# Kernel tuning notes

Measured on AMD Instinct MI355X. Metric: run time of the kernel, lower is better.

The kernel has to match this reference:

```python
import jax, jax.numpy as jnp
import numpy as np

DEPTH = 3
WIDTH = 512
WIDTH_SUB = 256
B = 64
L = 512
EPS = 1e-5
C_IN = 2 * WIDTH_SUB  # == WIDTH here, so per-depth params stack uniformly


def setup_inputs() -> dict:
    key = jax.random.key(0)
    ks = jax.random.split(key, 4)
    s = 1.0 / np.sqrt(C_IN).astype(np.float32)
    P_matrix = jax.random.normal(ks[0], (B, C_IN, L), jnp.float32)
    Wq = jax.random.normal(ks[1], (DEPTH, WIDTH, C_IN), jnp.float32) * s
    Wk = jax.random.normal(ks[2], (DEPTH, WIDTH, C_IN), jnp.float32) * s
    Wv = jax.random.normal(ks[3], (DEPTH, WIDTH, C_IN), jnp.float32) * s
    zeros = jnp.zeros((DEPTH, WIDTH), jnp.float32)
    ones = jnp.ones((DEPTH, WIDTH), jnp.float32)
    return {
        "P_matrix": P_matrix,
        "Wq": Wq, "bq": zeros, "gq": ones, "betaq": zeros,
        "Wk": Wk, "bk": zeros, "gk": ones, "betak": zeros,
        "Wv": Wv, "bv": zeros, "gv": ones, "betav": zeros,
    }


def _ncl_linear(x, W, b, gamma, beta):
    # x: [B, C, L]; Linear over channel dim, then BatchNorm1d (training stats) + ReLU
    y = jnp.einsum('bcl,oc->bol', x, W) + b[None, :, None]  # [B, O, L]
    mean = y.mean(axis=(0, 2), keepdims=True)
    var = y.var(axis=(0, 2), keepdims=True)  # biased, as torch BN uses for normalization
    y = (y - mean) * jax.lax.rsqrt(var + EPS) * gamma[None, :, None] + beta[None, :, None]
    return jax.nn.relu(y)


def reference(P_matrix, Wq, bq, gq, betaq, Wk, bk, gk, betak, Wv, bv, gv, betav):
    x = P_matrix
    for i in range(DEPTH):
        Q = _ncl_linear(x, Wq[i], bq[i], gq[i], betaq[i])  # [B, W, L]
        K = _ncl_linear(x, Wk[i], bk[i], gk[i], betak[i])
        V = _ncl_linear(x, Wv[i], bv[i], gv[i], betav[i])
        w = jnp.einsum('bcl,bdl->bcd', Q, K)  # [B, W, W], unscaled
        # nn.Softmax() with dim=None on a 3D tensor -> dim=0 in torch
        a = jax.nn.softmax(w, axis=0)
        x = jnp.einsum('bcd,bdl->bcl', a, V)  # [B, W, L]
    return x
```

## Files before the change

### kernel.cpp

```cpp
#include <hip/hip_runtime.h>
#include <hip/hip_fp8.h>
#include <stdint.h>

typedef __bf16 bf16_t;
typedef bf16_t bf16x8 __attribute__((ext_vector_type(8)));
typedef bf16_t bf16x4 __attribute__((ext_vector_type(4)));
typedef float  f32x4  __attribute__((ext_vector_type(4)));

#define MFMA_BF16(a,b,c) __builtin_amdgcn_mfma_f32_16x16x32_bf16(a,b,c,0,0,0)

__device__ __forceinline__ void load_lds16(const bf16_t* g, bf16_t* l) {
  __builtin_amdgcn_global_load_lds((const __attribute__((address_space(1))) void*)g,
                                   (__attribute__((address_space(3))) void*)l,
                                   16, 0, 0);
}

__device__ __forceinline__ float fp8_to_f(uint8_t b) {
  return (float)__builtin_bit_cast(__hip_fp8_e4m3, b);
}
__device__ __forceinline__ uint8_t f_to_fp8(float f) {
  return __builtin_bit_cast(uint8_t, __hip_fp8_e4m3(f));
}
__device__ __forceinline__ uint8_t fp8s_enc(float r) { return f_to_fp8(r * 256.f); }
__device__ __forceinline__ float   fp8s_dec(uint8_t b) { return fp8_to_f(b) * (1.f/256.f); }

__global__ __launch_bounds__(256) void cast_w_kern(const float* __restrict__ wq,
    const float* __restrict__ wk, const float* __restrict__ wv,
    bf16_t* __restrict__ whi, bf16_t* __restrict__ wlo) {
  const int i = blockIdx.x * 256 + threadIdx.x;
  const int idx = i * 4;
  const int p = idx / 786432;
  const int r = idx - p * 786432;
  const float* s = (p == 0 ? wq : (p == 1 ? wk : wv));
  float4 v = *(const float4*)(s + r);
  float f[4] = {v.x, v.y, v.z, v.w};
  bf16x4 hi, lo;
#pragma unroll
  for (int j = 0; j < 4; ++j) {
    bf16_t h = (bf16_t)f[j];
    hi[j] = h;
    lo[j] = (bf16_t)(f[j] - (float)h);
  }
  const size_t o = (size_t)p * 786432 + r;
  *(bf16x4*)(whi + o) = hi;
  *(bf16x4*)(wlo + o) = lo;
}

__global__ __launch_bounds__(256) void transpose_split_in_kern(
    const float* __restrict__ P, bf16_t* __restrict__ xh, uint8_t* __restrict__ xl) {
  __shared__ float t[32][33];
  const int bz = blockIdx.x >> 8;
  const int ti = blockIdx.x & 255;
  const int tc = (ti >> 4) * 32;
  const int tl = (ti & 15) * 32;
  const float* Pb = P + (size_t)bz * 262144;
  bf16_t* xb = xh + (size_t)bz * 262144;
  uint8_t* lb = xl + (size_t)bz * 262144;
  const int tx = threadIdx.x & 31, ty = threadIdx.x >> 5;
#pragma unroll
  for (int k = 0; k < 4; ++k)
    t[ty*4+k][tx] = Pb[(size_t)(tc + ty*4 + k)*512 + tl + tx];
  __syncthreads();
#pragma unroll
  for (int k = 0; k < 4; ++k) {
    const float f = t[tx][ty*4+k];
    const bf16_t h = (bf16_t)f;
    const size_t o = (size_t)(tl + ty*4 + k)*512 + tc + tx;
    xb[o] = h;
    lb[o] = fp8s_enc(f - (float)h);
  }
}

__global__ __launch_bounds__(256) void gemm_qkv_kern(
    const bf16_t* __restrict__ Whi, const bf16_t* __restrict__ Wlo,
    const bf16_t* __restrict__ xh, const uint8_t* __restrict__ xl,
    const float* __restrict__ bq, const float* __restrict__ bk,
    const float* __restrict__ bv, int depth,
    bf16_t* __restrict__ Qh, uint8_t* __restrict__ Ql,
    bf16_t* __restrict__ Kh, uint8_t* __restrict__ Kl,
    bf16_t* __restrict__ Yvh, bf16_t* __restrict__ Yvl) {
  __shared__ __align__(16) bf16_t Ah[4096], Al[4096], Bh[4096], Bl[4096];
  const int blk = blockIdx.x;
  const int t  = blk & 15;
  const int pb = blk >> 4;
  const int b  = pb & 63, p = pb >> 6;
  const int row0 = (t >> 2) * 128, col0 = (t & 3) * 128;
  const size_t woff = (size_t)p * 786432 + (size_t)depth * 262144;
  const bf16_t* A_hi = Whi + woff;
  const bf16_t* A_lo = Wlo + woff;
  const bf16_t* B_hi = xh + (size_t)b * 262144;
  const uint8_t* B_lo = xl + (size_t)b * 262144;
  const int tid = threadIdx.x, lane = tid & 63, wid = tid >> 6;
  const int wm = wid >> 1, wn = wid & 1;
  const int sr = tid >> 2, scs = (tid & 3) * 8;
  const int frow = lane & 15, fk = (lane >> 4) * 8;
  const int lrow = tid >> 1, lhalf = (tid & 1) * 16;
  f32x4 acc[4][4] = {};
  bf16_t* lah = Ah + wid * 512;
  bf16_t* lal = Al + wid * 512;
  bf16_t* lbh = Bh + wid * 512;
  const bf16_t* gah = A_hi + (size_t)(row0 + sr) * 512 + scs;
  const bf16_t* gal = A_lo + (size_t)(row0 + sr) * 512 + scs;
  const bf16_t* gbh = B_hi + (size_t)(col0 + sr) * 512 + scs;
  const uint8_t* gbl = B_lo + (size_t)(col0 + lrow) * 512 + lhalf;
  for (int ks = 0; ks < 16; ++ks) {
    const int k0 = ks * 32;
    load_lds16(gah + k0, lah); load_lds16(gah + 32768 + k0, lah + 2048);
    load_lds16(gal + k0, lal); load_lds16(gal + 32768 + k0, lal + 2048);
    load_lds16(gbh + k0, lbh); load_lds16(gbh + 32768 + k0, lbh + 2048);
    {
      uint4 raw = *(const uint4*)(gbl + k0);
      uint8_t by[16]; *(uint4*)by = raw;
      bf16x8 v0, v1;
#pragma unroll
      for (int j = 0; j < 8; ++j) v0[j] = (bf16_t)fp8s_dec(by[j]);
#pragma unroll
      for (int j = 0; j < 8; ++j) v1[j] = (bf16_t)fp8s_dec(by[8+j]);
      *(bf16x8*)(Bl + lrow*32 + lhalf)     = v0;
      *(bf16x8*)(Bl + lrow*32 + lhalf + 8) = v1;
    }
    __syncthreads();
    bf16x8 ah[4], al[4], bh[4], bl[4];
#pragma unroll
    for (int i = 0; i < 4; ++i) {
      const int ai = (wm*64 + i*16 + frow)*32 + fk;
      const int bi = (wn*64 + i*16 + frow)*32 + fk;
      ah[i] = *(const bf16x8*)(Ah + ai);
      al[i] = *(const bf16x8*)(Al + ai);
      bh[i] = *(const bf16x8*)(Bh + bi);
      bl[i] = *(const bf16x8*)(Bl + bi);
    }
#pragma unroll
    for (int i = 0; i < 4; ++i)
#pragma unroll
      for (int j = 0; j < 4; ++j) {
        acc[i][j] = MFMA_BF16(ah[i], bh[j], acc[i][j]);
        acc[i][j] = MFMA_BF16(al[i], bh[j], acc[i][j]);
        acc[i][j] = MFMA_BF16(ah[i], bl[j], acc[i][j]);
      }
    __syncthreads();
  }
  const float* bias = (p == 0 ? bq : (p == 1 ? bk : bv)) + depth * 512;
  if (p < 2) {
    bf16_t* Oh = (p == 0 ? Qh : Kh) + (size_t)b * 262144;
    uint8_t* Ol = (p == 0 ? Ql : Kl) + (size_t)b * 262144;
#pragma unroll
    for (int i = 0; i < 4; ++i)
#pragma unroll
      for (int j = 0; j < 4; ++j)
#pragma unroll
        for (int r = 0; r < 4; ++r) {
          const int rr = row0 + wm*64 + i*16 + (lane >> 4)*4 + r;
          const int cc = col0 + wn*64 + j*16 + (lane & 15);
          const float y = acc[i][j][r] + bias[rr];
          const bf16_t h = (bf16_t)y;
          Oh[(size_t)rr * 512 + cc] = h;
          Ol[(size_t)rr * 512 + cc] = fp8s_enc(y - (float)h);
        }
  } else {
    bf16_t* Ovh = Yvh + (size_t)b * 262144;
    bf16_t* Ovl = Yvl + (size_t)b * 262144;
#pragma unroll
    for (int i = 0; i < 4; ++i)
#pragma unroll
      for (int j = 0; j < 4; ++j)
#pragma unroll
        for (int r = 0; r < 4; ++r) {
          const int rr = row0 + wm*64 + i*16 + (lane >> 4)*4 + r;
          const int cc = col0 + wn*64 + j*16 + (lane & 15);
          const float y = acc[i][j][r] + bias[rr];
          const bf16_t h = (bf16_t)y;
          Ovh[(size_t)rr * 512 + cc] = h;
          Ovl[(size_t)rr * 512 + cc] = (bf16_t)(y - (float)h);
        }
  }
}

__global__ __launch_bounds__(256) void bn_stats_kern(
    const bf16_t* __restrict__ Qh, const bf16_t* __restrict__ Kh,
    const bf16_t* __restrict__ Yvh,
    const float* __restrict__ gq, const float* __restrict__ gk, const float* __restrict__ gv,
    const float* __restrict__ betaq, const float* __restrict__ betak, const float* __restrict__ betav,
    int depth, float* __restrict__ scale, float* __restrict__ shift) {
  const int po = blockIdx.x;
  const int p = po >> 9, o = po & 511;
  const bf16_t* base = (p == 0 ? Qh : (p == 1 ? Kh : Yvh)) + (size_t)o * 512;
  float s = 0.f, ss = 0.f;
  const int tid = threadIdx.x;
  for (int i = tid; i < 8192; i += 256) {
    const int b = i >> 7;
    const int l4 = (i & 127) * 4;
    bf16x4 v = *(const bf16x4*)(base + (size_t)b * 262144 + l4);
#pragma unroll
    for (int j = 0; j < 4; ++j) { float f = (float)v[j]; s += f; ss += f * f; }
  }
#pragma unroll
  for (int off = 32; off > 0; off >>= 1) {
    s  += __shfl_down(s, off);
    ss += __shfl_down(ss, off);
  }
  __shared__ float rs[4], rss[4];
  const int lane = tid & 63, wid = tid >> 6;
  if (lane == 0) { rs[wid] = s; rss[wid] = ss; }
  __syncthreads();
  if (tid == 0) {
    const float S  = rs[0] + rs[1] + rs[2] + rs[3];
    const float SS = rss[0] + rss[1] + rss[2] + rss[3];
    const float mean = S * (1.f / 32768.f);
    float var = SS * (1.f / 32768.f) - mean * mean;
    var = fmaxf(var, 0.f);
    const float* gp = (p == 0 ? gq : (p == 1 ? gk : gv));
    const float* bp = (p == 0 ? betaq : (p == 1 ? betak : betav));
    const float gamma = gp[depth * 512 + o];
    const float beta  = bp[depth * 512 + o];
    const float sc = gamma * rsqrtf(var + 1e-5f);
    scale[po] = sc;
    shift[po] = beta - mean * sc;
  }
}

__global__ __launch_bounds__(256) void norm_qk_kern(
    bf16_t* __restrict__ Qh, uint8_t* __restrict__ Ql,
    bf16_t* __restrict__ Kh, uint8_t* __restrict__ Kl,
    const float* __restrict__ scale, const float* __restrict__ shift) {
  const size_t i = ((size_t)blockIdx.x * 256 + threadIdx.x) * 4;
  const int p = (int)(i >> 24);
  const size_t j = i & 0xFFFFFF;
  const int o = (int)(j >> 9) & 511;
  const int po = p * 512 + o;
  const float sc = scale[po], sh = shift[po];
  bf16_t* H = (p == 0 ? Qh : Kh) + j;
  uint8_t* L = (p == 0 ? Ql : Kl) + j;
  bf16x4 hv = *(bf16x4*)H;
  uint32_t lv = *(uint32_t*)L;
  bf16x4 ho;
  uint32_t lo_out = 0;
#pragma unroll
  for (int k = 0; k < 4; ++k) {
    const float y = (float)hv[k] + fp8s_dec((uint8_t)(lv >> (8*k)));
    const float q = fmaxf(y * sc + sh, 0.f);
    const bf16_t h = (bf16_t)q;
    ho[k] = h;
    lo_out |= (uint32_t)fp8s_enc(q - (float)h) << (8*k);
  }
  *(bf16x4*)H = ho;
  *(uint32_t*)L = lo_out;
}

__global__ __launch_bounds__(256) void norm_v_t_kern(
    const bf16_t* __restrict__ Yvh, const bf16_t* __restrict__ Yvl,
    const float* __restrict__ scale, const float* __restrict__ shift,
    bf16_t* __restrict__ VTh, uint8_t* __restrict__ VTl) {
  __shared__ float t[32][33];
  const int bz = blockIdx.x >> 8;
  const int ti = blockIdx.x & 255;
  const int td = (ti >> 4) * 32;
  const int tl = (ti & 15) * 32;
  const size_t boff = (size_t)bz * 262144;
  const int tx = threadIdx.x & 31, ty = threadIdx.x >> 5;
#pragma unroll
  for (int k = 0; k < 4; ++k) {
    const int dd = td + ty*4 + k;
    const float sc = scale[1024 + dd], sh = shift[1024 + dd];
    const size_t o = boff + (size_t)dd * 512 + tl + tx;
    const float f = (float)Yvh[o] + (float)Yvl[o];
    t[ty*4+k][tx] = fmaxf(f * sc + sh, 0.f);
  }
  __syncthreads();
#pragma unroll
  for (int k = 0; k < 4; ++k) {
    const float v = t[tx][ty*4+k];
    const bf16_t h = (bf16_t)v;
    const size_t o = boff + (size_t)(tl + ty*4 + k)*512 + td + tx;
    VTh[o] = h;
    VTl[o] = fp8s_enc(v - (float)h);
  }
}

__global__ __launch_bounds__(256) void gemm_w_kern(
    const bf16_t* __restrict__ Qh, const uint8_t* __restrict__ Ql,
    const bf16_t* __restrict__ Kh, const uint8_t* __restrict__ Kl,
    float* __restrict__ w) {
  __shared__ __align__(16) bf16_t Ah[4096], Al[4096], Bh[4096], Bl[4096];
  const int blk = blockIdx.x;
  const int t = blk & 15;
  const int b = blk >> 4;
  const int row0 = (t >> 2) * 128, col0 = (t & 3) * 128;
  const bf16_t* A_hi = Qh + (size_t)b * 262144;
  const uint8_t* A_lo = Ql + (size_t)b * 262144;
  const bf16_t* B_hi = Kh + (size_t)b * 262144;
  const uint8_t* B_lo = Kl + (size_t)b * 262144;
  const int tid = threadIdx.x, lane = tid & 63, wid = tid >> 6;
  const int wm = wid >> 1, wn = wid & 1;
  const int sr = tid >> 2, scs = (tid & 3) * 8;
  const int frow = lane & 15, fk = (lane >> 4) * 8;
  const int lrow = tid >> 1, lhalf = (tid & 1) * 16;
  f32x4 acc[4][4] = {};
  bf16_t* lah = Ah + wid * 512;
  bf16_t* lbh = Bh + wid * 512;
  const bf16_t* gah = A_hi + (size_t)(row0 + sr) * 512 + scs;
  const bf16_t* gbh = B_hi + (size_t)(col0 + sr) * 512 + scs;
  const uint8_t* gal = A_lo + (size_t)(row0 + lrow) * 512 + lhalf;
  const uint8_t* gbl = B_lo + (size_t)(col0 + lrow) * 512 + lhalf;
  for (int ks = 0; ks < 16; ++ks) {
    const int k0 = ks * 32;
    load_lds16(gah + k0, lah); load_lds16(gah + 32768 + k0, lah + 2048);
    load_lds16(gbh + k0, lbh); load_lds16(gbh + 32768 + k0, lbh + 2048);
    {
      uint4 ra = *(const uint4*)(gal + k0);
      uint4 rb = *(const uint4*)(gbl + k0);
      uint8_t ba[16]; *(uint4*)ba = ra;
      uint8_t bb[16]; *(uint4*)bb = rb;
      bf16x8 a0, a1, b0, b1;
#pragma unroll
      for (int j = 0; j < 8; ++j) { a0[j] = (bf16_t)fp8s_dec(ba[j]); a1[j] = (bf16_t)fp8s_dec(ba[8+j]); }
#pragma unroll
      for (int j = 0; j < 8; ++j) { b0[j] = (bf16_t)fp8s_dec(bb[j]); b1[j] = (bf16_t)fp8s_dec(bb[8+j]); }
      *(bf16x8*)(Al + lrow*32 + lhalf)     = a0;
      *(bf16x8*)(Al + lrow*32 + lhalf + 8) = a1;
      *(bf16x8*)(Bl + lrow*32 + lhalf)     = b0;
      *(bf16x8*)(Bl + lrow*32 + lhalf + 8) = b1;
    }
    __syncthreads();
    bf16x8 ah[4], al[4], bh[4], bl[4];
#pragma unroll
    for (int i = 0; i < 4; ++i) {
      const int ai = (wm*64 + i*16 + frow)*32 + fk;
      const int bi = (wn*64 + i*16 + frow)*32 + fk;
      ah[i] = *(const bf16x8*)(Ah + ai);
      al[i] = *(const bf16x8*)(Al + ai);
      bh[i] = *(const bf16x8*)(Bh + bi);
      bl[i] = *(const bf16x8*)(Bl + bi);
    }
#pragma unroll
    for (int i = 0; i < 4; ++i)
#pragma unroll
      for (int j = 0; j < 4; ++j) {
        acc[i][j] = MFMA_BF16(ah[i], bh[j], acc[i][j]);
        acc[i][j] = MFMA_BF16(al[i], bh[j], acc[i][j]);
        acc[i][j] = MFMA_BF16(ah[i], bl[j], acc[i][j]);
      }
    __syncthreads();
  }
  float* wb = w + (size_t)b * 262144;
#pragma unroll
  for (int i = 0; i < 4; ++i)
#pragma unroll
    for (int j = 0; j < 4; ++j)
#pragma unroll
      for (int r = 0; r < 4; ++r) {
        const int rr = row0 + wm*64 + i*16 + (lane >> 4)*4 + r;
        const int cc = col0 + wn*64 + j*16 + (lane & 15);
        wb[(size_t)rr * 512 + cc] = acc[i][j][r];
      }
}

__global__ __launch_bounds__(256) void softmax_kern(float* __restrict__ w) {
  const int idx = blockIdx.x * 256 + threadIdx.x;
  float v[64];
#pragma unroll
  for (int b = 0; b < 64; ++b) v[b] = w[idx + (size_t)b * 262144];
  float m = v[0];
#pragma unroll
  for (int b = 1; b < 64; ++b) m = fmaxf(m, v[b]);
  float s = 0.f;
#pragma unroll
  for (int b = 0; b < 64; ++b) { v[b] = __expf(v[b] - m); s += v[b]; }
  const float inv = 1.f / s;
#pragma unroll
  for (int b = 0; b < 64; ++b) w[idx + (size_t)b * 262144] = v[b] * inv;
}

__global__ __launch_bounds__(256) void gemm_x_kern(
    const bf16_t* __restrict__ VTh, const uint8_t* __restrict__ VTl,
    const float* __restrict__ a,
    bf16_t* __restrict__ xh, uint8_t* __restrict__ xl) {
  __shared__ __align__(16) bf16_t Ah[4096], Al[4096], Bh[4096], Bl[4096];
  const int blk = blockIdx.x;
  const int t = blk & 15;
  const int b = blk >> 4;
  const int row0 = (t >> 2) * 128, col0 = (t & 3) * 128;
  const bf16_t* Ahg = VTh + (size_t)b * 262144;
  const uint8_t* Alg = VTl + (size_t)b * 262144;
  const float*   Bg  = a   + (size_t)b * 262144;
  const int tid = threadIdx.x, lane = tid & 63, wid = tid >> 6;
  const int wm = wid >> 1, wn = wid & 1;
  const int sr = tid >> 2, scs = (tid & 3) * 8;
  const int frow = lane & 15, fk = (lane >> 4) * 8;
  const int lrow = tid >> 1, lhalf = (tid & 1) * 16;
  f32x4 acc[4][4] = {};
  bf16_t* lah = Ah + wid * 512;
  const bf16_t* gah = Ahg + (size_t)(row0 + sr) * 512 + scs;
  const uint8_t* gal = Alg + (size_t)(row0 + lrow) * 512 + lhalf;
  for (int ks = 0; ks < 16; ++ks) {
    const int k0 = ks * 32;
    load_lds16(gah + k0, lah); load_lds16(gah + 32768 + k0, lah + 2048);
    {
      uint4 raw = *(const uint4*)(gal + k0);
      uint8_t by[16]; *(uint4*)by = raw;
      bf16x8 v0, v1;
#pragma unroll
      for (int j = 0; j < 8; ++j) v0[j] = (bf16_t)fp8s_dec(by[j]);
#pragma unroll
      for (int j = 0; j < 8; ++j) v1[j] = (bf16_t)fp8s_dec(by[8+j]);
      *(bf16x8*)(Al + lrow*32 + lhalf)     = v0;
      *(bf16x8*)(Al + lrow*32 + lhalf + 8) = v1;
    }
    {
#pragma unroll
      for (int p = 0; p < 4; ++p) {
        const int idx = p * 256 + tid;
        const int br = idx >> 3;
        const int cs = (idx & 7) * 4;
        float4 v4 = *(const float4*)(Bg + (size_t)(col0 + br) * 512 + k0 + cs);
        float f[4] = {v4.x, v4.y, v4.z, v4.w};
        bf16x4 hv, lv;
#pragma unroll
        for (int j = 0; j < 4; ++j) {
          bf16_t h = (bf16_t)f[j];
          hv[j] = h;
          lv[j] = (bf16_t)(f[j] - (float)h);
        }
        *(bf16x4*)(Bh + br*32 + cs) = hv;
        *(bf16x4*)(Bl + br*32 + cs) = lv;
      }
    }
    __syncthreads();
    bf16x8 ah[4], al[4], bh[4], bl[4];
#pragma unroll
    for (int i = 0; i < 4; ++i) {
      const int ai = (wm*64 + i*16 + frow)*32 + fk;
      const int bi = (wn*64 + i*16 + frow)*32 + fk;
      ah[i] = *(const bf16x8*)(Ah + ai);
      al[i] = *(const bf16x8*)(Al + ai);
      bh[i] = *(const bf16x8*)(Bh + bi);
      bl[i] = *(const bf16x8*)(Bl + bi);
    }
#pragma unroll
    for (int i = 0; i < 4; ++i)
#pragma unroll
      for (int j = 0; j < 4; ++j) {
        acc[i][j] = MFMA_BF16(ah[i], bh[j], acc[i][j]);
        acc[i][j] = MFMA_BF16(al[i], bh[j], acc[i][j]);
        acc[i][j] = MFMA_BF16(ah[i], bl[j], acc[i][j]);
      }
    __syncthreads();
  }
  bf16_t* xb = xh + (size_t)b * 262144;
  uint8_t* lb8 = xl + (size_t)b * 262144;
#pragma unroll
  for (int i = 0; i < 4; ++i)
#pragma unroll
    for (int j = 0; j < 4; ++j)
#pragma unroll
      for (int r = 0; r < 4; ++r) {
        const int rr = row0 + wm*64 + i*16 + (lane >> 4)*4 + r;
        const int cc = col0 + wn*64 + j*16 + (lane & 15);
        const float y = acc[i][j][r];
        const bf16_t h = (bf16_t)y;
        xb[(size_t)rr * 512 + cc] = h;
        lb8[(size_t)rr * 512 + cc] = fp8s_enc(y - (float)h);
      }
}

__global__ __launch_bounds__(256) void out_transpose_kern(
    const bf16_t* __restrict__ xh, const uint8_t* __restrict__ xl,
    float* __restrict__ out) {
  __shared__ float t[32][33];
  const int bz = blockIdx.x >> 8;
  const int ti = blockIdx.x & 255;
  const int tl = (ti >> 4) * 32;
  const int tc = (ti & 15) * 32;
  const bf16_t* xb = xh + (size_t)bz * 262144;
  const uint8_t* lb = xl + (size_t)bz * 262144;
  float* ob = out + (size_t)bz * 262144;
  const int tx = threadIdx.x & 31, ty = threadIdx.x >> 5;
#pragma unroll
  for (int k = 0; k < 4; ++k) {
    const size_t o = (size_t)(tl + ty*4 + k)*512 + tc + tx;
    t[ty*4+k][tx] = (float)xb[o] + fp8s_dec(lb[o]);
  }
  __syncthreads();
#pragma unroll
  for (int k = 0; k < 4; ++k)
    ob[(size_t)(tc + ty*4 + k)*512 + tl + tx] = t[tx][ty*4+k];
}

extern "C" void kernel_launch(void* const* d_in, const int* in_sizes, int n_in,
                              void* d_out, int out_size, void* d_ws, size_t ws_size,
                              hipStream_t stream) {
  const float* P     = (const float*)d_in[0];
  const float* Wq    = (const float*)d_in[1];
  const float* bq    = (const float*)d_in[2];
  const float* gq    = (const float*)d_in[3];
  const float* betaq = (const float*)d_in[4];
  const float* Wk    = (const float*)d_in[5];
  const float* bk    = (const float*)d_in[6];
  const float* gk    = (const float*)d_in[7];
  const float* betak = (const float*)d_in[8];
  const float* Wv    = (const float*)d_in[9];
  const float* bv    = (const float*)d_in[10];
  const float* gv    = (const float*)d_in[11];
  const float* betav = (const float*)d_in[12];

  char* ws = (char*)d_ws;
  size_t off = 0;
  auto alloc = [&](size_t bytes) -> char* {
    char* p = ws + off;
    off += (bytes + 255) & ~(size_t)255;
    return p;
  };
  bf16_t*  Sh[3]; uint8_t* Sl[3];
  for (int i = 0; i < 3; ++i) {
    Sh[i] = (bf16_t*) alloc(33554432);
    Sl[i] = (uint8_t*)alloc(16777216);
  }
  char* E = alloc(67108864);
  float*  w   = (float*)E;
  bf16_t* Yvh = (bf16_t*)E;
  bf16_t* Yvl = (bf16_t*)(E + 33554432);
  bf16_t* Whi = (bf16_t*)alloc(4718592);
  bf16_t* Wlo = (bf16_t*)alloc(4718592);
  float* scale = (float*)alloc(6144);
  float* shift = (float*)alloc(6144);

  cast_w_kern<<<2304, 256, 0, stream>>>(Wq, Wk, Wv, Whi, Wlo);
  transpose_split_in_kern<<<16384, 256, 0, stream>>>(P, Sh[0], Sl[0]);
  for (int d = 0; d < 3; ++d) {
    const int xi = (d == 1) ? 1 : 0;
    const int qi = (d == 1) ? 0 : 1;
    const int ki = 2;
    const int ni = (d == 2) ? 2 : qi;
    gemm_qkv_kern<<<3072, 256, 0, stream>>>(Whi, Wlo, Sh[xi], Sl[xi],
        bq, bk, bv, d, Sh[qi], Sl[qi], Sh[ki], Sl[ki], Yvh, Yvl);
    bn_stats_kern<<<1536, 256, 0, stream>>>(Sh[qi], Sh[ki], Yvh,
        gq, gk, gv, betaq, betak, betav, d, scale, shift);
    norm_qk_kern<<<32768, 256, 0, stream>>>(Sh[qi], Sl[qi], Sh[ki], Sl[ki],
        scale, shift);
    norm_v_t_kern<<<16384, 256, 0, stream>>>(Yvh, Yvl, scale, shift,
        Sh[xi], Sl[xi]);
    gemm_w_kern<<<1024, 256, 0, stream>>>(Sh[qi], Sl[qi], Sh[ki], Sl[ki], w);
    softmax_kern<<<1024, 256, 0, stream>>>(w);
    gemm_x_kern<<<1024, 256, 0, stream>>>(Sh[xi], Sl[xi], w, Sh[ni], Sl[ni]);
  }
  out_transpose_kern<<<16384, 256, 0, stream>>>(Sh[2], Sl[2], (float*)d_out);
}
```

Before: 1.472 ms.

## Fuse BatchNorm statistics into QKV GEMM epilogue with atomics; retile fp8 low loads

The QKV GEMM epilogue now reduces per-channel sum and sum of squares across lanes and adds them into global accumulators with atomics. This replaces the separate bn_stats pass, which reread all Q/K/V high parts, with a tiny finalize kernel that computes scale/shift and clears the accumulators. Statistics now come from fp32 values rather than the bf16 high part, and the atomics make the summation order nondeterministic. Separately, the fp8 low-part loads in the three GEMMs switch to two 8-byte loads per thread matching the bf16 tile mapping, decoded through a shared helper.

Result: slower. 1.718 ms (+16.7%).

```diff
diff --git a/kernel.cpp b/kernel.cpp
--- a/kernel.cpp
+++ b/kernel.cpp
@@ -23,6 +23,13 @@
 }
 __device__ __forceinline__ uint8_t fp8s_enc(float r) { return f_to_fp8(r * 256.f); }
 __device__ __forceinline__ float   fp8s_dec(uint8_t b) { return fp8_to_f(b) * (1.f/256.f); }
+
+__device__ __forceinline__ bf16x8 dec8(uint64_t v) {
+  bf16x8 o;
+#pragma unroll
+  for (int j = 0; j < 8; ++j) o[j] = (bf16_t)fp8s_dec((uint8_t)(v >> (8*j)));
+  return o;
+}
 
 __global__ __launch_bounds__(256) void cast_w_kern(const float* __restrict__ wq,
     const float* __restrict__ wk, const float* __restrict__ wv,
@@ -78,7 +85,8 @@
     const float* __restrict__ bv, int depth,
     bf16_t* __restrict__ Qh, uint8_t* __restrict__ Ql,
     bf16_t* __restrict__ Kh, uint8_t* __restrict__ Kl,
-    bf16_t* __restrict__ Yvh, bf16_t* __restrict__ Yvl) {
+    bf16_t* __restrict__ Yvh, bf16_t* __restrict__ Yvl,
+    float* __restrict__ bsum, float* __restrict__ bsum2) {
   __shared__ __align__(16) bf16_t Ah[4096], Al[4096], Bh[4096], Bl[4096];
   const int blk = blockIdx.x;
   const int t  = blk & 15;
@@ -94,7 +102,6 @@
   const int wm = wid >> 1, wn = wid & 1;
   const int sr = tid >> 2, scs = (tid & 3) * 8;
   const int frow = lane & 15, fk = (lane >> 4) * 8;
-  const int lrow = tid >> 1, lhalf = (tid & 1) * 16;
   f32x4 acc[4][4] = {};
   bf16_t* lah = Ah + wid * 512;
   bf16_t* lal = Al + wid * 512;
@@ -102,22 +109,17 @@
   const bf16_t* gah = A_hi + (size_t)(row0 + sr) * 512 + scs;
   const bf16_t* gal = A_lo + (size_t)(row0 + sr) * 512 + scs;
   const bf16_t* gbh = B_hi + (size_t)(col0 + sr) * 512 + scs;
-  const uint8_t* gbl = B_lo + (size_t)(col0 + lrow) * 512 + lhalf;
+  const uint8_t* gbl = B_lo + (size_t)(col0 + sr) * 512 + scs;
   for (int ks = 0; ks < 16; ++ks) {
     const int k0 = ks * 32;
     load_lds16(gah + k0, lah); load_lds16(gah + 32768 + k0, lah + 2048);
     load_lds16(gal + k0, lal); load_lds16(gal + 32768 + k0, lal + 2048);
     load_lds16(gbh + k0, lbh); load_lds16(gbh + 32768 + k0, lbh + 2048);
     {
-      uint4 raw = *(const uint4*)(gbl + k0);
-      uint8_t by[16]; *(uint4*)by = raw;
-      bf16x8 v0, v1;
-#pragma unroll
-      for (int j = 0; j < 8; ++j) v0[j] = (bf16_t)fp8s_dec(by[j]);
-#pragma unroll
-      for (int j = 0; j < 8; ++j) v1[j] = (bf16_t)fp8s_dec(by[8+j]);
-      *(bf16x8*)(Bl + lrow*32 + lhalf)     = v0;
-      *(bf16x8*)(Bl + lrow*32 + lhalf + 8) = v1;
+      const uint64_t r0 = *(const uint64_t*)(gbl + k0);
+      const uint64_t r1 = *(const uint64_t*)(gbl + 32768 + k0);
+      *(bf16x8*)(Bl + sr*32 + scs)        = dec8(r0);
+      *(bf16x8*)(Bl + 2048 + sr*32 + scs) = dec8(r1);
     }
     __syncthreads();
     bf16x8 ah[4], al[4], bh[4], bl[4];
@@ -147,76 +149,80 @@
 #pragma unroll
     for (int i = 0; i < 4; ++i)
 #pragma unroll
-      for (int j = 0; j < 4; ++j)
-#pragma unroll
-        for (int r = 0; r < 4; ++r) {
-          const int rr = row0 + wm*64 + i*16 + (lane >> 4)*4 + r;
+      for (int r = 0; r < 4; ++r) {
+        const int rr = row0 + wm*64 + i*16 + (lane >> 4)*4 + r;
+        const float bb = bias[rr];
+        float s = 0.f, ss = 0.f;
+#pragma unroll
+        for (int j = 0; j < 4; ++j) {
           const int cc = col0 + wn*64 + j*16 + (lane & 15);
-          const float y = acc[i][j][r] + bias[rr];
+          const float y = acc[i][j][r] + bb;
+          s += y; ss += y * y;
           const bf16_t h = (bf16_t)y;
           Oh[(size_t)rr * 512 + cc] = h;
           Ol[(size_t)rr * 512 + cc] = fp8s_enc(y - (float)h);
         }
+#pragma unroll
+        for (int m = 1; m < 16; m <<= 1) {
+          s  += __shfl_xor(s, m);
+          ss += __shfl_xor(ss, m);
+        }
+        if ((lane & 15) == 0) {
+          atomicAdd(&bsum[p * 512 + rr], s);
+          atomicAdd(&bsum2[p * 512 + rr], ss);
+        }
+      }
   } else {
     bf16_t* Ovh = Yvh + (size_t)b * 262144;
     bf16_t* Ovl = Yvl + (size_t)b * 262144;
 #pragma unroll
     for (int i = 0; i < 4; ++i)
 #pragma unroll
-      for (int j = 0; j < 4; ++j)
-#pragma unroll
-        for (int r = 0; r < 4; ++r) {
-          const int rr = row0 + wm*64 + i*16 + (lane >> 4)*4 + r;
+      for (int r = 0; r < 4; ++r) {
+        const int rr = row0 + wm*64 + i*16 + (lane >> 4)*4 + r;
+        const float bb = bias[rr];
+        float s = 0.f, ss = 0.f;
+#pragma unroll
+        for (int j = 0; j < 4; ++j) {
           const int cc = col0 + wn*64 + j*16 + (lane & 15);
-          const float y = acc[i][j][r] + bias[rr];
+          const float y = acc[i][j][r] + bb;
+          s += y; ss += y * y;
           const bf16_t h = (bf16_t)y;
           Ovh[(size_t)rr * 512 + cc] = h;
           Ovl[(size_t)rr * 512 + cc] = (bf16_t)(y - (float)h);
         }
-  }
-}
-
-__global__ __launch_bounds__(256) void bn_stats_kern(
-    const bf16_t* __restrict__ Qh, const bf16_t* __restrict__ Kh,
-    const bf16_t* __restrict__ Yvh,
+#pragma unroll
+        for (int m = 1; m < 16; m <<= 1) {
+          s  += __shfl_xor(s, m);
+          ss += __shfl_xor(ss, m);
+        }
+        if ((lane & 15) == 0) {
+          atomicAdd(&bsum[1024 + rr], s);
+          atomicAdd(&bsum2[1024 + rr], ss);
+        }
+      }
+  }
+}
+
+__global__ __launch_bounds__(256) void bn_finalize_kern(
+    float* __restrict__ bsum, float* __restrict__ bsum2,
     const float* __restrict__ gq, const float* __restrict__ gk, const float* __restrict__ gv,
     const float* __restrict__ betaq, const float* __restrict__ betak, const float* __restrict__ betav,
     int depth, float* __restrict__ scale, float* __restrict__ shift) {
-  const int po = blockIdx.x;
+  const int po = blockIdx.x * 256 + threadIdx.x;
   const int p = po >> 9, o = po & 511;
-  const bf16_t* base = (p == 0 ? Qh : (p == 1 ? Kh : Yvh)) + (size_t)o * 512;
-  float s = 0.f, ss = 0.f;
-  const int tid = threadIdx.x;
-  for (int i = tid; i < 8192; i += 256) {
-    const int b = i >> 7;
-    const int l4 = (i & 127) * 4;
-    bf16x4 v = *(const bf16x4*)(base + (size_t)b * 262144 + l4);
-#pragma unroll
-    for (int j = 0; j < 4; ++j) { float f = (float)v[j]; s += f; ss += f * f; }
-  }
-#pragma unroll
-  for (int off = 32; off > 0; off >>= 1) {
-    s  += __shfl_down(s, off);
-    ss += __shfl_down(ss, off);
-  }
-  __shared__ float rs[4], rss[4];
-  const int lane = tid & 63, wid = tid >> 6;
-  if (lane == 0) { rs[wid] = s; rss[wid] = ss; }
-  __syncthreads();
-  if (tid == 0) {
-    const float S  = rs[0] + rs[1] + rs[2] + rs[3];
-    const float SS = rss[0] + rss[1] + rss[2] + rss[3];
-    const float mean = S * (1.f / 32768.f);
-    float var = SS * (1.f / 32768.f) - mean * mean;
-    var = fmaxf(var, 0.f);
-    const float* gp = (p == 0 ? gq : (p == 1 ? gk : gv));
-    const float* bp = (p == 0 ? betaq : (p == 1 ? betak : betav));
-    const float gamma = gp[depth * 512 + o];
-    const float beta  = bp[depth * 512 + o];
-    const float sc = gamma * rsqrtf(var + 1e-5f);
-    scale[po] = sc;
-    shift[po] = beta - mean * sc;
-  }
+  const float mean = bsum[po] * (1.f / 32768.f);
+  float var = bsum2[po] * (1.f / 32768.f) - mean * mean;
+  var = fmaxf(var, 0.f);
+  const float* gp = (p == 0 ? gq : (p == 1 ? gk : gv));
+  const float* bp = (p == 0 ? betaq : (p == 1 ? betak : betav));
+  const float gamma = gp[depth * 512 + o];
+  const float beta  = bp[depth * 512 + o];
+  const float sc = gamma * rsqrtf(var + 1e-5f);
+  scale[po] = sc;
+  shift[po] = beta - mean * sc;
+  bsum[po] = 0.f;
+  bsum2[po] = 0.f;
 }
 
 __global__ __launch_bounds__(256) void norm_qk_kern(
@@ -294,32 +300,26 @@
   const int wm = wid >> 1, wn = wid & 1;
   const int sr = tid >> 2, scs = (tid & 3) * 8;
   const int frow = lane & 15, fk = (lane >> 4) * 8;
-  const int lrow = tid >> 1, lhalf = (tid & 1) * 16;
   f32x4 acc[4][4] = {};
   bf16_t* lah = Ah + wid * 512;
   bf16_t* lbh = Bh + wid * 512;
   const bf16_t* gah = A_hi + (size_t)(row0 + sr) * 512 + scs;
   const bf16_t* gbh = B_hi + (size_t)(col0 + sr) * 512 + scs;
-  const uint8_t* gal = A_lo + (size_t)(row0 + lrow) * 512 + lhalf;
-  const uint8_t* gbl = B_lo + (size_t)(col0 + lrow) * 512 + lhalf;
+  const uint8_t* gal = A_lo + (size_t)(row0 + sr) * 512 + scs;
+  const uint8_t* gbl = B_lo + (size_t)(col0 + sr) * 512 + scs;
   for (int ks = 0; ks < 16; ++ks) {
     const int k0 = ks * 32;
     load_lds16(gah + k0, lah); load_lds16(gah + 32768 + k0, lah + 2048);
     load_lds16(gbh + k0, lbh); load_lds16(gbh + 32768 + k0, lbh + 2048);
     {
-      uint4 ra = *(const uint4*)(gal + k0);
-      uint4 rb = *(const uint4*)(gbl + k0);
-      uint8_t ba[16]; *(uint4*)ba = ra;
-      uint8_t bb[16]; *(uint4*)bb = rb;
-      bf16x8 a0, a1, b0, b1;
-#pragma unroll
-      for (int j = 0; j < 8; ++j) { a0[j] = (bf16_t)fp8s_dec(ba[j]); a1[j] = (bf16_t)fp8s_dec(ba[8+j]); }
-#pragma unroll
-      for (int j = 0; j < 8; ++j) { b0[j] = (bf16_t)fp8s_dec(bb[j]); b1[j] = (bf16_t)fp8s_dec(bb[8+j]); }
-      *(bf16x8*)(Al + lrow*32 + lhalf)     = a0;
-      *(bf16x8*)(Al + lrow*32 + lhalf + 8) = a1;
-      *(bf16x8*)(Bl + lrow*32 + lhalf)     = b0;
-      *(bf16x8*)(Bl + lrow*32 + lhalf + 8) = b1;
+      const uint64_t ra0 = *(const uint64_t*)(gal + k0);
+      const uint64_t ra1 = *(const uint64_t*)(gal + 32768 + k0);
+      const uint64_t rb0 = *(const uint64_t*)(gbl + k0);
+      const uint64_t rb1 = *(const uint64_t*)(gbl + 32768 + k0);
+      *(bf16x8*)(Al + sr*32 + scs)        = dec8(ra0);
+      *(bf16x8*)(Al + 2048 + sr*32 + scs) = dec8(ra1);
+      *(bf16x8*)(Bl + sr*32 + scs)        = dec8(rb0);
+      *(bf16x8*)(Bl + 2048 + sr*32 + scs) = dec8(rb1);
     }
     __syncthreads();
     bf16x8 ah[4], al[4], bh[4], bl[4];
@@ -387,24 +387,18 @@
   const int wm = wid >> 1, wn = wid & 1;
   const int sr = tid >> 2, scs = (tid & 3) * 8;
   const int frow = lane & 15, fk = (lane >> 4) * 8;
-  const int lrow = tid >> 1, lhalf = (tid & 1) * 16;
   f32x4 acc[4][4] = {};
   bf16_t* lah = Ah + wid * 512;
   const bf16_t* gah = Ahg + (size_t)(row0 + sr) * 512 + scs;
-  const uint8_t* gal = Alg + (size_t)(row0 + lrow) * 512 + lhalf;
+  const uint8_t* gal = Alg + (size_t)(row0 + sr) * 512 + scs;
   for (int ks = 0; ks < 16; ++ks) {
     const int k0 = ks * 32;
     load_lds16(gah + k0, lah); load_lds16(gah + 32768 + k0, lah + 2048);
     {
-      uint4 raw = *(const uint4*)(gal + k0);
-      uint8_t by[16]; *(uint4*)by = raw;
-      bf16x8 v0, v1;
-#pragma unroll
-      for (int j = 0; j < 8; ++j) v0[j] = (bf16_t)fp8s_dec(by[j]);
-#pragma unroll
-      for (int j = 0; j < 8; ++j) v1[j] = (bf16_t)fp8s_dec(by[8+j]);
-      *(bf16x8*)(Al + lrow*32 + lhalf)     = v0;
-      *(bf16x8*)(Al + lrow*32 + lhalf + 8) = v1;
+      const uint64_t r0 = *(const uint64_t*)(gal + k0);
+      const uint64_t r1 = *(const uint64_t*)(gal + 32768 + k0);
+      *(bf16x8*)(Al + sr*32 + scs)        = dec8(r0);
+      *(bf16x8*)(Al + 2048 + sr*32 + scs) = dec8(r1);
     }
     {
 #pragma unroll
@@ -523,7 +517,10 @@
   bf16_t* Wlo = (bf16_t*)alloc(4718592);
   float* scale = (float*)alloc(6144);
   float* shift = (float*)alloc(6144);
-
+  float* bsum  = (float*)alloc(6144);
+  float* bsum2 = (float*)alloc(6144);
+
+  hipMemsetAsync(bsum, 0, 12288, stream);
   cast_w_kern<<<2304, 256, 0, stream>>>(Wq, Wk, Wv, Whi, Wlo);
   transpose_split_in_kern<<<16384, 256, 0, stream>>>(P, Sh[0], Sl[0]);
   for (int d = 0; d < 3; ++d) {
@@ -532,9 +529,9 @@
     const int ki = 2;
     const int ni = (d == 2) ? 2 : qi;
     gemm_qkv_kern<<<3072, 256, 0, stream>>>(Whi, Wlo, Sh[xi], Sl[xi],
-        bq, bk, bv, d, Sh[qi], Sl[qi], Sh[ki], Sl[ki], Yvh, Yvl);
-    bn_stats_kern<<<1536, 256, 0, stream>>>(Sh[qi], Sh[ki], Yvh,
-        gq, gk, gv, betaq, betak, betav, d, scale, shift);
+        bq, bk, bv, d, Sh[qi], Sl[qi], Sh[ki], Sl[ki], Yvh, Yvl, bsum, bsum2);
+    bn_finalize_kern<<<6, 256, 0, stream>>>(bsum, bsum2, gq, gk, gv,
+        betaq, betak, betav, d, scale, shift);
     norm_qk_kern<<<32768, 256, 0, stream>>>(Sh[qi], Sl[qi], Sh[ki], Sl[ki],
         scale, shift);
     norm_v_t_kern<<<16384, 256, 0, stream>>>(Yvh, Yvl, scale, shift,
```
